# Kernel optimization log

Hardware: AMD Instinct MI355X
Metric: run time of the kernel (lower is better)

Reference implementation:

```python
import jax, jax.numpy as jnp
import numpy as np

N_HEADS = 16
N_KV_HEADS = 4
N_EMBD = 1024

def setup_inputs() -> dict:
    key = jax.random.key(0)
    kx, kq, kk, kv, ko = jax.random.split(key, 5)
    B, S, E = 2, 2048, N_EMBD
    head_dim = E // N_HEADS
    kv_dim = N_KV_HEADS * head_dim  # 256
    scale = 0.02
    return {
        "x": jax.random.normal(kx, (B, S, E), dtype=jnp.float32),
        "Wq": jax.random.normal(kq, (E, E), dtype=jnp.float32) * scale,
        "Wk": jax.random.normal(kk, (E, kv_dim), dtype=jnp.float32) * scale,
        "Wv": jax.random.normal(kv, (E, kv_dim), dtype=jnp.float32) * scale,
        "Wo": jax.random.normal(ko, (E, E), dtype=jnp.float32) * scale,
    }

def reference(x, Wq, Wk, Wv, Wo):
    B, S, E = x.shape
    H, KV = N_HEADS, N_KV_HEADS
    D = E // H            # head_dim = 64
    R = H // KV           # query heads per kv head = 4
    inv_sqrt_d = 1.0 / (D ** 0.5)

    q = (x @ Wq).reshape(B, S, KV, R, D)   # group query heads by kv group
    k = (x @ Wk).reshape(B, S, KV, D)
    v = (x @ Wv).reshape(B, S, KV, D)

    # repeat_interleave(kv, R, dim=heads) == broadcast kv head g to query heads (g, r)
    scores = jnp.einsum('bqgrd,bkgd->bgrqk', q, k) * inv_sqrt_d  # [B,KV,R,S,S]
    causal = jnp.tril(jnp.ones((S, S), dtype=bool))
    scores = jnp.where(causal, scores, jnp.float32(-jnp.inf))
    attn = jax.nn.softmax(scores, axis=-1)

    out = jnp.einsum('bgrqk,bkgd->bqgrd', attn, v).reshape(B, S, E)
    return out @ Wo
```

## Files before the change

### kernel.cpp

```cpp
#include <hip/hip_runtime.h>
#include <hip/hip_bf16.h>

#define B_SZ   2
#define S_LEN  2048
#define E_DIM  1024
#define H_Q    16
#define H_KV   4
#define HD     64
#define KV_DIM 256
#define M_ROWS (B_SZ * S_LEN)
#define N_QT   (S_LEN / 64)

typedef short bf16x4 __attribute__((ext_vector_type(4)));
typedef short bf16x8 __attribute__((ext_vector_type(8)));
typedef float f32x4  __attribute__((ext_vector_type(4)));
typedef unsigned u32x2 __attribute__((ext_vector_type(2)));

#define MFMA16x32(a, b, c) __builtin_amdgcn_mfma_f32_16x16x32_bf16(a, b, c, 0, 0, 0)

#if __has_builtin(__builtin_amdgcn_mfma_f32_16x16x16bf16_1k)
#define MFMA_PV(a, b, c) __builtin_amdgcn_mfma_f32_16x16x16bf16_1k(a, b, c, 0, 0, 0)
#elif __has_builtin(__builtin_amdgcn_mfma_f32_16x16x16_bf16)
#define MFMA_PV(a, b, c) __builtin_amdgcn_mfma_f32_16x16x16_bf16(a, b, c, 0, 0, 0)
#else
static __device__ inline f32x4 mfma_pv_asm(bf16x4 a, bf16x4 b, f32x4 c) {
    asm volatile("v_mfma_f32_16x16x16_bf16 %0, %1, %2, %0"
                 : "+v"(c) : "v"(a), "v"(b));
    return c;
}
#define MFMA_PV(a, b, c) mfma_pv_asm(a, b, c)
#endif

static __device__ __forceinline__ short f32_to_bf16(float f) {
    unsigned u = __builtin_bit_cast(unsigned, f);
    u += 0x7fffu + ((u >> 16) & 1u);
    return (short)(u >> 16);
}

static __device__ __forceinline__ unsigned pack2_trunc(float a, float b) {
    unsigned ua = __builtin_bit_cast(unsigned, a);
    unsigned ub = __builtin_bit_cast(unsigned, b);
    return (ua >> 16) | (ub & 0xffff0000u);
}

static __device__ __forceinline__ void load_lds16(const short* g, short* l) {
    __builtin_amdgcn_global_load_lds(
        (const __attribute__((address_space(1))) void*)g,
        (__attribute__((address_space(3))) void*)l, 16, 0, 0);
}

__device__ __forceinline__ void transpose_body(const float* __restrict__ W,
                                               short* __restrict__ Wt,
                                               int K, int N, int bx, int by) {
    __shared__ float t[32][33];
    const int n0 = bx * 32, k0 = by * 32;
    const int tx = threadIdx.x & 31, ty = threadIdx.x >> 5;
#pragma unroll
    for (int i = 0; i < 32; i += 8)
        t[ty + i][tx] = W[(long)(k0 + ty + i) * N + n0 + tx];
    __syncthreads();
#pragma unroll
    for (int i = 0; i < 32; i += 8)
        Wt[(long)(n0 + ty + i) * K + k0 + tx] = f32_to_bf16(t[tx][ty + i]);
}

__global__ __launch_bounds__(256)
void prep(const float* __restrict__ x,
          const float* __restrict__ Wq, const float* __restrict__ Wk,
          const float* __restrict__ Wv, const float* __restrict__ Wo,
          short* __restrict__ xbf, short* __restrict__ Wqt,
          short* __restrict__ Wkt, short* __restrict__ Wvt,
          short* __restrict__ Wot) {
    const int bid = blockIdx.x;
    if (bid < 4096) {
        const int i = bid * 256 + threadIdx.x;
        float4 v = ((const float4*)x)[i];
        bf16x4 o;
        o[0] = f32_to_bf16(v.x); o[1] = f32_to_bf16(v.y);
        o[2] = f32_to_bf16(v.z); o[3] = f32_to_bf16(v.w);
        ((bf16x4*)xbf)[i] = o;
    } else if (bid < 5120) {
        const int r = bid - 4096;
        transpose_body(Wq, Wqt, E_DIM, E_DIM, r & 31, r >> 5);
    } else if (bid < 5376) {
        const int r = bid - 5120;
        transpose_body(Wk, Wkt, E_DIM, KV_DIM, r & 7, r >> 3);
    } else if (bid < 5632) {
        const int r = bid - 5376;
        transpose_body(Wv, Wvt, E_DIM, KV_DIM, r & 7, r >> 3);
    } else {
        const int r = bid - 5632;
        transpose_body(Wo, Wot, E_DIM, E_DIM, r & 31, r >> 5);
    }
}

__device__ __forceinline__ void gemm64x128(const short* __restrict__ Ab,
                                           const short* __restrict__ Btb,
                                           int K, short* As, short* Bs,
                                           f32x4 acc[2][4]) {
    const int tid  = threadIdx.x;
    const int wave = tid >> 6;
    const int lane = tid & 63;
    const int lq   = lane & 15;
    const int lg   = lane >> 4;
    const int wm   = wave >> 1;
    const int wn   = wave & 1;
    const int lrow = lane >> 2;
    const int lkc  = (lane & 3) * 8;

#pragma unroll
    for (int i = 0; i < 2; ++i)
#pragma unroll
        for (int j = 0; j < 4; ++j) acc[i][j] = (f32x4){0.f, 0.f, 0.f, 0.f};

    for (int k0 = 0; k0 < K; k0 += 32) {
        __syncthreads();
        {
            const int m0 = wave * 16;
            load_lds16(Ab + (size_t)(m0 + lrow) * K + k0 + lkc, As + m0 * 32);
        }
#pragma unroll
        for (int it = 0; it < 2; ++it) {
            const int m0 = wave * 32 + it * 16;
            load_lds16(Btb + (size_t)(m0 + lrow) * K + k0 + lkc, Bs + m0 * 32);
        }
        __syncthreads();
        bf16x8 af[2], bfr[4];
#pragma unroll
        for (int i = 0; i < 2; ++i)
            af[i] = *(const bf16x8*)&As[(wm * 32 + i * 16 + lq) * 32 + lg * 8];
#pragma unroll
        for (int j = 0; j < 4; ++j)
            bfr[j] = *(const bf16x8*)&Bs[(wn * 64 + j * 16 + lq) * 32 + lg * 8];
#pragma unroll
        for (int i = 0; i < 2; ++i)
#pragma unroll
            for (int j = 0; j < 4; ++j)
                acc[i][j] = MFMA16x32(af[i], bfr[j], acc[i][j]);
    }
}

__global__ __launch_bounds__(256)
void qkv_gemm(const short* __restrict__ xbf,
              const short* __restrict__ Wqt, const short* __restrict__ Wkt,
              const short* __restrict__ Wvt,
              short* __restrict__ Qbf, short* __restrict__ Kbf,
              short* __restrict__ Vbf, float qscale) {
    __shared__ short As[64 * 32];
    __shared__ short Bs[128 * 32];
    const int nb = blockIdx.x;
    const int mb = blockIdx.y;
    const short* Bt; short* out; int ldc, ncol0; float alpha;
    if (nb < 8) {
        Bt = Wqt + (size_t)nb * 128 * E_DIM;
        out = Qbf; ldc = E_DIM; ncol0 = nb * 128; alpha = qscale;
    } else if (nb < 10) {
        Bt = Wkt + (size_t)(nb - 8) * 128 * E_DIM;
        out = Kbf; ldc = KV_DIM; ncol0 = (nb - 8) * 128; alpha = 1.f;
    } else {
        Bt = Wvt + (size_t)(nb - 10) * 128 * E_DIM;
        out = Vbf; ldc = KV_DIM; ncol0 = (nb - 10) * 128; alpha = 1.f;
    }
    f32x4 acc[2][4];
    gemm64x128(xbf + (size_t)mb * 64 * E_DIM, Bt, E_DIM, As, Bs, acc);

    const int lane = threadIdx.x & 63, wave = threadIdx.x >> 6;
    const int lq = lane & 15, lg = lane >> 4, wm = wave >> 1, wn = wave & 1;
#pragma unroll
    for (int i = 0; i < 2; ++i)
#pragma unroll
        for (int r = 0; r < 4; ++r) {
            const size_t row = (size_t)mb * 64 + wm * 32 + i * 16 + lg * 4 + r;
#pragma unroll
            for (int j = 0; j < 4; ++j)
                out[row * ldc + ncol0 + wn * 64 + j * 16 + lq] =
                    f32_to_bf16(acc[i][j][r] * alpha);
        }
}

__global__ __launch_bounds__(256)
void gemm_o(const short* __restrict__ Abf, const short* __restrict__ Wot,
            float* __restrict__ C) {
    __shared__ short As[64 * 32];
    __shared__ short Bs[128 * 32];
    const int nb = blockIdx.x;
    const int mb = blockIdx.y;
    f32x4 acc[2][4];
    gemm64x128(Abf + (size_t)mb * 64 * E_DIM,
               Wot + (size_t)nb * 128 * E_DIM, E_DIM, As, Bs, acc);

    const int lane = threadIdx.x & 63, wave = threadIdx.x >> 6;
    const int lq = lane & 15, lg = lane >> 4, wm = wave >> 1, wn = wave & 1;
#pragma unroll
    for (int i = 0; i < 2; ++i)
#pragma unroll
        for (int r = 0; r < 4; ++r) {
            const size_t row = (size_t)mb * 64 + wm * 32 + i * 16 + lg * 4 + r;
#pragma unroll
            for (int j = 0; j < 4; ++j)
                C[row * E_DIM + nb * 128 + wn * 64 + j * 16 + lq] =
                    acc[i][j][r];
        }
}

struct KVregs { bf16x8 k[2], v[2]; };

__device__ __forceinline__ void stage_load(const short* __restrict__ Kb,
                                           const short* __restrict__ Vb,
                                           long rowbase, int g, KVregs& kv) {
    const int tid = threadIdx.x;
#pragma unroll
    for (int it = 0; it < 2; ++it) {
        const int c   = tid + it * 256;
        const int row = c >> 3;
        const int ch  = c & 7;
        const long src = (rowbase + row) * KV_DIM + g * HD + ch * 8;
        kv.k[it] = *(const bf16x8*)(Kb + src);
        kv.v[it] = *(const bf16x8*)(Vb + src);
    }
}

__device__ __forceinline__ void stage_write(short (*Ks)[72], short (*Vt)[70],
                                            const KVregs& kv) {
    const int tid = threadIdx.x;
#pragma unroll
    for (int it = 0; it < 2; ++it) {
        const int c   = tid + it * 256;
        const int row = c >> 3;
        const int ch  = c & 7;
        *(bf16x8*)&Ks[row][ch * 8] = kv.k[it];
#pragma unroll
        for (int i = 0; i < 8; ++i) Vt[ch * 8 + i][row] = kv.v[it][i];
    }
}

__global__ __launch_bounds__(256)
void flash_mfma(const short* __restrict__ Qb,
                const short* __restrict__ Kb,
                const short* __restrict__ Vb,
                short* __restrict__ Ob) {
    const int pair = blockIdx.x;
    const int h    = blockIdx.y;
    const int b    = blockIdx.z;
    const int g    = h >> 2;

    const int tid  = threadIdx.x;
    const int wave = tid >> 6;
    const int lane = tid & 63;
    const int lq   = lane & 15;
    const int lg   = lane >> 4;

    __shared__ short Ks[2][64][72];
    __shared__ short Vt[2][64][70];

    for (int rep = 0; rep < 2; ++rep) {
        const int qt = rep ? (N_QT - 1 - pair) : pair;
        const int qs = qt * 64;

        const short* qrow =
            Qb + ((long)(b * S_LEN + qs + wave * 16 + lq)) * E_DIM + h * HD;
        const bf16x8 qf0 = *(const bf16x8*)(qrow + lg * 8);
        const bf16x8 qf1 = *(const bf16x8*)(qrow + 32 + lg * 8);

        f32x4 o[4];
#pragma unroll
        for (int dc = 0; dc < 4; ++dc) o[dc] = (f32x4){0.f, 0.f, 0.f, 0.f};
        float l_run = 0.f;

        KVregs kv;
        stage_load(Kb, Vb, (long)b * S_LEN, g, kv);
        stage_write(Ks[0], Vt[0], kv);
        __syncthreads();

        int p = 0;
        for (int kt = 0; kt <= qt; ++kt) {
            if (kt < qt)
                stage_load(Kb, Vb, (long)b * S_LEN + (kt + 1) * 64, g, kv);

            const int cmax = (kt == qt) ? wave : 3;
            f32x4 s[4];
#pragma unroll
            for (int c = 0; c < 4; ++c) {
                if (c > cmax) continue;
                bf16x8 kf0 = *(const bf16x8*)&Ks[p][c * 16 + lq][lg * 8];
                bf16x8 kf1 = *(const bf16x8*)&Ks[p][c * 16 + lq][32 + lg * 8];
                f32x4 acc = (f32x4){0.f, 0.f, 0.f, 0.f};
                acc = MFMA16x32(kf0, qf0, acc);
                acc = MFMA16x32(kf1, qf1, acc);
                s[c] = acc;
            }

            if (kt == qt) {
#pragma unroll
                for (int r = 0; r < 4; ++r)
                    if (lg * 4 + r > lq) s[wave][r] = -INFINITY;
            }

            float psum = 0.f;
#pragma unroll
            for (int c = 0; c < 4; ++c) {
                if (c > cmax) continue;
#pragma unroll
                for (int r = 0; r < 4; ++r) {
                    float pe = exp2f(s[c][r]);
                    s[c][r] = pe;
                    psum += pe;
                }
            }
            l_run += psum;

#pragma unroll
            for (int c = 0; c < 4; ++c) {
                if (c > cmax) continue;
                u32x2 packed;
                packed[0] = pack2_trunc(s[c][0], s[c][1]);
                packed[1] = pack2_trunc(s[c][2], s[c][3]);
                bf16x4 pa = __builtin_bit_cast(bf16x4, packed);
#pragma unroll
                for (int dc = 0; dc < 4; ++dc) {
                    bf16x4 vf =
                        *(const bf16x4*)&Vt[p][dc * 16 + lq][c * 16 + lg * 4];
                    o[dc] = MFMA_PV(pa, vf, o[dc]);
                }
            }

            if (kt < qt) stage_write(Ks[p ^ 1], Vt[p ^ 1], kv);
            __syncthreads();
            p ^= 1;
        }

        l_run += __shfl_xor(l_run, 16);
        l_run += __shfl_xor(l_run, 32);

#pragma unroll
        for (int r = 0; r < 4; ++r) {
            const float lT  = __shfl(l_run, lg * 4 + r);
            const float inv = 1.f / lT;
            const long base =
                ((long)(b * S_LEN + qs + wave * 16 + lg * 4 + r)) * E_DIM +
                h * HD + lq;
#pragma unroll
            for (int dc = 0; dc < 4; ++dc)
                Ob[base + dc * 16] = f32_to_bf16(o[dc][r] * inv);
        }
    }
}

extern "C" void kernel_launch(void* const* d_in, const int* in_sizes, int n_in,
                              void* d_out, int out_size, void* d_ws, size_t ws_size,
                              hipStream_t stream) {
    const float* x  = (const float*)d_in[0];
    const float* Wq = (const float*)d_in[1];
    const float* Wk = (const float*)d_in[2];
    const float* Wv = (const float*)d_in[3];
    const float* Wo = (const float*)d_in[4];
    float* out = (float*)d_out;

    short* xbf = (short*)d_ws;
    short* Wqt = xbf + (size_t)M_ROWS * E_DIM;
    short* Wkt = Wqt + (size_t)E_DIM * E_DIM;
    short* Wvt = Wkt + (size_t)KV_DIM * E_DIM;
    short* Wot = Wvt + (size_t)KV_DIM * E_DIM;
    short* Qbf = Wot + (size_t)E_DIM * E_DIM;
    short* Kbf = Qbf + (size_t)M_ROWS * E_DIM;
    short* Vbf = Kbf + (size_t)M_ROWS * KV_DIM;
    short* Abf = Vbf + (size_t)M_ROWS * KV_DIM;

    const float qscale = 0.125f * 1.44269504088896340736f;

    prep<<<dim3(6656), dim3(256), 0, stream>>>(
        x, Wq, Wk, Wv, Wo, xbf, Wqt, Wkt, Wvt, Wot);
    qkv_gemm<<<dim3(12, M_ROWS / 64), dim3(256), 0, stream>>>(
        xbf, Wqt, Wkt, Wvt, Qbf, Kbf, Vbf, qscale);
    flash_mfma<<<dim3(N_QT / 2, H_Q, B_SZ), dim3(256), 0, stream>>>(
        Qbf, Kbf, Vbf, Abf);
    gemm_o<<<dim3(E_DIM / 128, M_ROWS / 64), dim3(256), 0, stream>>>(
        Abf, Wot, out);
}
```

Measured before the change: 182.0 us.

## Pre-transpose V globally and enlarge GEMM tiles to 128x128

Adds a transpose_v kernel that writes V in a [group,batch,d,seq] layout, so the flash kernel can store V tiles into LDS with vector writes instead of per-element scattered transposed stores. Separately, the QKV and output GEMMs move from 64x128 to 128x128 block tiles with 4x4 MFMA accumulators per wave, doubling A-tile reuse. The cost is an extra kernel launch and workspace buffer, higher register pressure, and half as many GEMM blocks, which may underfill the GPU's compute units.

```diff
diff --git a/kernel.cpp b/kernel.cpp
--- a/kernel.cpp
+++ b/kernel.cpp
@@ -94,10 +94,36 @@
     }
 }
 
-__device__ __forceinline__ void gemm64x128(const short* __restrict__ Ab,
-                                           const short* __restrict__ Btb,
-                                           int K, short* As, short* Bs,
-                                           f32x4 acc[2][4]) {
+__global__ __launch_bounds__(256)
+void transpose_v(const short* __restrict__ V, short* __restrict__ Vt) {
+    const int st = blockIdx.x;
+    const int gb = blockIdx.y;
+    const int g  = gb >> 1, b = gb & 1;
+    const int s0 = st * 64;
+    __shared__ short Ls[64][72];
+#pragma unroll
+    for (int it = 0; it < 2; ++it) {
+        const int slot = threadIdx.x + it * 256;
+        const int si = slot >> 3, ch = slot & 7;
+        *(bf16x8*)&Ls[si][ch * 8] = *(const bf16x8*)
+            &V[((long)(b * S_LEN + s0 + si)) * KV_DIM + g * HD + ch * 8];
+    }
+    __syncthreads();
+#pragma unroll
+    for (int it = 0; it < 2; ++it) {
+        const int slot = threadIdx.x + it * 256;
+        const int d = slot >> 3, ch = slot & 7;
+        bf16x8 v;
+#pragma unroll
+        for (int i = 0; i < 8; ++i) v[i] = Ls[ch * 8 + i][d];
+        *(bf16x8*)&Vt[((long)(gb * HD + d)) * S_LEN + s0 + ch * 8] = v;
+    }
+}
+
+__device__ __forceinline__ void gemm128(const short* __restrict__ Ab,
+                                        const short* __restrict__ Btb,
+                                        int K, short* As, short* Bs,
+                                        f32x4 acc[4][4]) {
     const int tid  = threadIdx.x;
     const int wave = tid >> 6;
     const int lane = tid & 63;
@@ -109,31 +135,28 @@
     const int lkc  = (lane & 3) * 8;
 
 #pragma unroll
-    for (int i = 0; i < 2; ++i)
+    for (int i = 0; i < 4; ++i)
 #pragma unroll
         for (int j = 0; j < 4; ++j) acc[i][j] = (f32x4){0.f, 0.f, 0.f, 0.f};
 
     for (int k0 = 0; k0 < K; k0 += 32) {
         __syncthreads();
-        {
-            const int m0 = wave * 16;
-            load_lds16(Ab + (size_t)(m0 + lrow) * K + k0 + lkc, As + m0 * 32);
-        }
 #pragma unroll
         for (int it = 0; it < 2; ++it) {
             const int m0 = wave * 32 + it * 16;
-            load_lds16(Btb + (size_t)(m0 + lrow) * K + k0 + lkc, Bs + m0 * 32);
+            const int m  = m0 + lrow;
+            load_lds16(Ab  + (size_t)m * K + k0 + lkc, As + m0 * 32);
+            load_lds16(Btb + (size_t)m * K + k0 + lkc, Bs + m0 * 32);
         }
         __syncthreads();
-        bf16x8 af[2], bfr[4];
-#pragma unroll
-        for (int i = 0; i < 2; ++i)
-            af[i] = *(const bf16x8*)&As[(wm * 32 + i * 16 + lq) * 32 + lg * 8];
-#pragma unroll
-        for (int j = 0; j < 4; ++j)
-            bfr[j] = *(const bf16x8*)&Bs[(wn * 64 + j * 16 + lq) * 32 + lg * 8];
-#pragma unroll
-        for (int i = 0; i < 2; ++i)
+        bf16x8 af[4], bfr[4];
+#pragma unroll
+        for (int i = 0; i < 4; ++i) {
+            af[i]  = *(const bf16x8*)&As[(wm * 64 + i * 16 + lq) * 32 + lg * 8];
+            bfr[i] = *(const bf16x8*)&Bs[(wn * 64 + i * 16 + lq) * 32 + lg * 8];
+        }
+#pragma unroll
+        for (int i = 0; i < 4; ++i)
 #pragma unroll
             for (int j = 0; j < 4; ++j)
                 acc[i][j] = MFMA16x32(af[i], bfr[j], acc[i][j]);
@@ -146,7 +169,7 @@
               const short* __restrict__ Wvt,
               short* __restrict__ Qbf, short* __restrict__ Kbf,
               short* __restrict__ Vbf, float qscale) {
-    __shared__ short As[64 * 32];
+    __shared__ short As[128 * 32];
     __shared__ short Bs[128 * 32];
     const int nb = blockIdx.x;
     const int mb = blockIdx.y;
@@ -161,16 +184,16 @@
         Bt = Wvt + (size_t)(nb - 10) * 128 * E_DIM;
         out = Vbf; ldc = KV_DIM; ncol0 = (nb - 10) * 128; alpha = 1.f;
     }
-    f32x4 acc[2][4];
-    gemm64x128(xbf + (size_t)mb * 64 * E_DIM, Bt, E_DIM, As, Bs, acc);
+    f32x4 acc[4][4];
+    gemm128(xbf + (size_t)mb * 128 * E_DIM, Bt, E_DIM, As, Bs, acc);
 
     const int lane = threadIdx.x & 63, wave = threadIdx.x >> 6;
     const int lq = lane & 15, lg = lane >> 4, wm = wave >> 1, wn = wave & 1;
 #pragma unroll
-    for (int i = 0; i < 2; ++i)
+    for (int i = 0; i < 4; ++i)
 #pragma unroll
         for (int r = 0; r < 4; ++r) {
-            const size_t row = (size_t)mb * 64 + wm * 32 + i * 16 + lg * 4 + r;
+            const size_t row = (size_t)mb * 128 + wm * 64 + i * 16 + lg * 4 + r;
 #pragma unroll
             for (int j = 0; j < 4; ++j)
                 out[row * ldc + ncol0 + wn * 64 + j * 16 + lq] =
@@ -181,21 +204,21 @@
 __global__ __launch_bounds__(256)
 void gemm_o(const short* __restrict__ Abf, const short* __restrict__ Wot,
             float* __restrict__ C) {
-    __shared__ short As[64 * 32];
+    __shared__ short As[128 * 32];
     __shared__ short Bs[128 * 32];
     const int nb = blockIdx.x;
     const int mb = blockIdx.y;
-    f32x4 acc[2][4];
-    gemm64x128(Abf + (size_t)mb * 64 * E_DIM,
-               Wot + (size_t)nb * 128 * E_DIM, E_DIM, As, Bs, acc);
+    f32x4 acc[4][4];
+    gemm128(Abf + (size_t)mb * 128 * E_DIM,
+            Wot + (size_t)nb * 128 * E_DIM, E_DIM, As, Bs, acc);
 
     const int lane = threadIdx.x & 63, wave = threadIdx.x >> 6;
     const int lq = lane & 15, lg = lane >> 4, wm = wave >> 1, wn = wave & 1;
 #pragma unroll
-    for (int i = 0; i < 2; ++i)
+    for (int i = 0; i < 4; ++i)
 #pragma unroll
         for (int r = 0; r < 4; ++r) {
-            const size_t row = (size_t)mb * 64 + wm * 32 + i * 16 + lg * 4 + r;
+            const size_t row = (size_t)mb * 128 + wm * 64 + i * 16 + lg * 4 + r;
 #pragma unroll
             for (int j = 0; j < 4; ++j)
                 C[row * E_DIM + nb * 128 + wn * 64 + j * 16 + lq] =
@@ -206,21 +229,23 @@
 struct KVregs { bf16x8 k[2], v[2]; };
 
 __device__ __forceinline__ void stage_load(const short* __restrict__ Kb,
-                                           const short* __restrict__ Vb,
-                                           long rowbase, int g, KVregs& kv) {
+                                           const short* __restrict__ Vtg,
+                                           long b, long ks, int g,
+                                           KVregs& kv) {
     const int tid = threadIdx.x;
 #pragma unroll
     for (int it = 0; it < 2; ++it) {
         const int c   = tid + it * 256;
         const int row = c >> 3;
         const int ch  = c & 7;
-        const long src = (rowbase + row) * KV_DIM + g * HD + ch * 8;
-        kv.k[it] = *(const bf16x8*)(Kb + src);
-        kv.v[it] = *(const bf16x8*)(Vb + src);
-    }
-}
-
-__device__ __forceinline__ void stage_write(short (*Ks)[72], short (*Vt)[70],
+        kv.k[it] = *(const bf16x8*)
+            &Kb[(b * S_LEN + ks + row) * KV_DIM + g * HD + ch * 8];
+        kv.v[it] = *(const bf16x8*)
+            &Vtg[((long)(g * 2 + b) * HD + row) * S_LEN + ks + ch * 8];
+    }
+}
+
+__device__ __forceinline__ void stage_write(short (*Ks)[72], short (*Vt)[72],
                                             const KVregs& kv) {
     const int tid = threadIdx.x;
 #pragma unroll
@@ -229,15 +254,14 @@
         const int row = c >> 3;
         const int ch  = c & 7;
         *(bf16x8*)&Ks[row][ch * 8] = kv.k[it];
-#pragma unroll
-        for (int i = 0; i < 8; ++i) Vt[ch * 8 + i][row] = kv.v[it][i];
+        *(bf16x8*)&Vt[row][ch * 8] = kv.v[it];
     }
 }
 
 __global__ __launch_bounds__(256)
 void flash_mfma(const short* __restrict__ Qb,
                 const short* __restrict__ Kb,
-                const short* __restrict__ Vb,
+                const short* __restrict__ Vtg,
                 short* __restrict__ Ob) {
     const int pair = blockIdx.x;
     const int h    = blockIdx.y;
@@ -251,7 +275,7 @@
     const int lg   = lane >> 4;
 
     __shared__ short Ks[2][64][72];
-    __shared__ short Vt[2][64][70];
+    __shared__ short Vt[2][64][72];
 
     for (int rep = 0; rep < 2; ++rep) {
         const int qt = rep ? (N_QT - 1 - pair) : pair;
@@ -268,14 +292,14 @@
         float l_run = 0.f;
 
         KVregs kv;
-        stage_load(Kb, Vb, (long)b * S_LEN, g, kv);
+        stage_load(Kb, Vtg, b, 0, g, kv);
         stage_write(Ks[0], Vt[0], kv);
         __syncthreads();
 
         int p = 0;
         for (int kt = 0; kt <= qt; ++kt) {
             if (kt < qt)
-                stage_load(Kb, Vb, (long)b * S_LEN + (kt + 1) * 64, g, kv);
+                stage_load(Kb, Vtg, b, (long)(kt + 1) * 64, g, kv);
 
             const int cmax = (kt == qt) ? wave : 3;
             f32x4 s[4];
@@ -365,15 +389,18 @@
     short* Kbf = Qbf + (size_t)M_ROWS * E_DIM;
     short* Vbf = Kbf + (size_t)M_ROWS * KV_DIM;
     short* Abf = Vbf + (size_t)M_ROWS * KV_DIM;
+    short* Vtg = Abf + (size_t)M_ROWS * E_DIM;
 
     const float qscale = 0.125f * 1.44269504088896340736f;
 
     prep<<<dim3(6656), dim3(256), 0, stream>>>(
         x, Wq, Wk, Wv, Wo, xbf, Wqt, Wkt, Wvt, Wot);
-    qkv_gemm<<<dim3(12, M_ROWS / 64), dim3(256), 0, stream>>>(
+    qkv_gemm<<<dim3(12, M_ROWS / 128), dim3(256), 0, stream>>>(
         xbf, Wqt, Wkt, Wvt, Qbf, Kbf, Vbf, qscale);
+    transpose_v<<<dim3(S_LEN / 64, B_SZ * H_KV), dim3(256), 0, stream>>>(
+        Vbf, Vtg);
     flash_mfma<<<dim3(N_QT / 2, H_Q, B_SZ), dim3(256), 0, stream>>>(
-        Qbf, Kbf, Vbf, Abf);
-    gemm_o<<<dim3(E_DIM / 128, M_ROWS / 64), dim3(256), 0, stream>>>(
+        Qbf, Kbf, Vtg, Abf);
+    gemm_o<<<dim3(E_DIM / 128, M_ROWS / 128), dim3(256), 0, stream>>>(
         Abf, Wot, out);
 }
```

Result: no change. 181.6 us (-0.2%).
